# Optimization experiments

Measured on AMD Instinct MI355X. Metric: run time of the kernel, lower is better.

## Reference

```python
import jax, jax.numpy as jnp
import numpy as np

N_NODES, N_EDGES = 50000, 800000
NODE_D, MSG_D, OUT_D = 128, 128, 128


def _linear_params(key, d_in, d_out):
    kw, _ = jax.random.split(key)
    W = jax.random.normal(kw, (d_in, d_out), jnp.float32) * np.float32(1.0 / np.sqrt(d_in))
    b = jnp.zeros((d_out,), jnp.float32)
    return W, b


def setup_inputs() -> dict:
    key = jax.random.key(0)
    ks = jax.random.split(key, 12)
    node_features = jax.random.normal(ks[0], (N_NODES, NODE_D), jnp.float32)
    src = jax.random.randint(ks[1], (N_EDGES,), 0, N_NODES, dtype=jnp.int32)
    dst = jax.random.randint(ks[2], (N_EDGES,), 0, N_NODES, dtype=jnp.int32)
    W_msg_1, b_msg_1 = _linear_params(ks[3], NODE_D, MSG_D)
    W_msg_2, b_msg_2 = _linear_params(ks[4], MSG_D, MSG_D)
    W_msg_3, b_msg_3 = _linear_params(ks[5], MSG_D, MSG_D)
    W_att_1, b_att_1 = _linear_params(ks[6], 2 * NODE_D, 1)
    W_att_2, b_att_2 = _linear_params(ks[7], 2 * NODE_D, 1)
    W_att_3, b_att_3 = _linear_params(ks[8], 2 * NODE_D, 1)
    W_c1, b_c1 = _linear_params(ks[9], MSG_D + NODE_D, OUT_D)
    W_c2, b_c2 = _linear_params(ks[10], OUT_D, OUT_D)
    return {
        'node_features': node_features, 'src': src, 'dst': dst,
        'W_msg_1': W_msg_1, 'b_msg_1': b_msg_1,
        'W_msg_2': W_msg_2, 'b_msg_2': b_msg_2,
        'W_msg_3': W_msg_3, 'b_msg_3': b_msg_3,
        'W_att_1': W_att_1, 'b_att_1': b_att_1,
        'W_att_2': W_att_2, 'b_att_2': b_att_2,
        'W_att_3': W_att_3, 'b_att_3': b_att_3,
        'W_c1': W_c1, 'b_c1': b_c1,
        'W_c2': W_c2, 'b_c2': b_c2,
    }


def reference(node_features, src, dst,
              W_msg_1, b_msg_1, W_msg_2, b_msg_2, W_msg_3, b_msg_3,
              W_att_1, b_att_1, W_att_2, b_att_2, W_att_3, b_att_3,
              W_c1, b_c1, W_c2, b_c2):
    # dropout(0.2) is identity in eval mode
    h = node_features                     # [N, D]
    N = h.shape[0]
    hs = h[src]                           # [E, D] gather source features
    hd = h[dst]                           # [E, D] gather dest features
    e = jnp.concatenate([hs, hd], axis=1)  # [E, 2D]

    # three per-edge scalar attention heads: exp(relu(linear))
    a1 = jnp.exp(jax.nn.relu(e @ W_att_1 + b_att_1))  # [E, 1]
    a2 = jnp.exp(jax.nn.relu(e @ W_att_2 + b_att_2))
    a3 = jnp.exp(jax.nn.relu(e @ W_att_3 + b_att_3))

    # per-destination normalizers (segment sums over incoming edges)
    att1 = jax.ops.segment_sum(a1, dst, num_segments=N)  # [N, 1]
    att2 = jax.ops.segment_sum(a2, dst, num_segments=N)
    att3 = jax.ops.segment_sum(a3, dst, num_segments=N)

    avg_a = (a1 / att1[dst] + a2 / att2[dst] + a3 / att3[dst]) / 3.0  # [E, 1]

    # gathered 3-layer MLP message, scaled by averaged attention
    m = avg_a * jax.nn.relu(
        jax.nn.relu(jax.nn.relu(hs @ W_msg_1 + b_msg_1) @ W_msg_2 + b_msg_2) @ W_msg_3 + b_msg_3
    )  # [E, M]

    # mean over incoming edges (nodes with no in-edges get 0, like DGL)
    deg = jax.ops.segment_sum(jnp.ones((src.shape[0], 1), h.dtype), dst, num_segments=N)
    h_neigh = jax.ops.segment_sum(m, dst, num_segments=N) / jnp.maximum(deg, 1.0)  # [N, M]

    hc = jnp.concatenate([h, h_neigh], axis=1)  # [N, D+M]
    out = jax.nn.relu(hc @ W_c1 + b_c1) @ W_c2 + b_c2  # [N, O]
    return out
```

## Files before the change

### kernel.cpp

```cpp
#include <hip/hip_runtime.h>

#define NDIM 128
#define NWPART 128
#define MAXBKT 1024

typedef __attribute__((ext_vector_type(8))) short s8v;
typedef __attribute__((ext_vector_type(4))) float f4v;

__device__ inline unsigned short f2bf_rne(float x) {
    unsigned u = __float_as_uint(x);
    unsigned r = u + 0x7FFFu + ((u >> 16) & 1u);
    return (unsigned short)(r >> 16);
}
__device__ inline float bf2f(unsigned short b) {
    return __uint_as_float(((unsigned)b) << 16);
}

__global__ __launch_bounds__(256) void k_front(const float* __restrict__ h,
                                               const float* __restrict__ Wa1,
                                               const float* __restrict__ Wa2,
                                               const float* __restrict__ Wa3,
                                               float* __restrict__ proj,
                                               unsigned short* __restrict__ hb,
                                               const float* __restrict__ w0,
                                               const float* __restrict__ w1,
                                               const float* __restrict__ w2,
                                               const float* __restrict__ w3,
                                               const float* __restrict__ w4,
                                               const float* __restrict__ w5,
                                               unsigned short* __restrict__ wtout,
                                               const int* __restrict__ dst,
                                               int* __restrict__ hist,
                                               int N, int E, int nbkt)
{
    __shared__ int lh[MAXBKT];
    int tid = threadIdx.x;
    int nbProj = (N + 15) >> 4;
    int bid = blockIdx.x;

    if (bid < 384) {
        const float* srcs[6] = {w0, w1, w2, w3, w4, w5};
        int mat = bid >> 6;
        int idx = (bid & 63) * 256 + tid;
        int j    = idx & 7;
        int lane = (idx >> 3) & 63;
        int ks   = (idx >> 9) & 3;
        int ct   = idx >> 11;
        int col  = ct * 16 + (lane & 15);
        int k    = ks * 32 + (lane >> 4) * 8 + j;
        wtout[(size_t)mat * 16384 + idx] = f2bf_rne(srcs[mat][k * 128 + col]);
        return;
    }
    bid -= 384;
    if (bid < nbProj) {
        int l = tid & 15;
        int n = bid * 16 + (tid >> 4);
        if (n >= N) return;
        int o = l * 8;
        float4 w1s0 = *(const float4*)(Wa1 + o),       w1s1 = *(const float4*)(Wa1 + o + 4);
        float4 w1d0 = *(const float4*)(Wa1 + 128 + o), w1d1 = *(const float4*)(Wa1 + 132 + o);
        float4 w2s0 = *(const float4*)(Wa2 + o),       w2s1 = *(const float4*)(Wa2 + o + 4);
        float4 w2d0 = *(const float4*)(Wa2 + 128 + o), w2d1 = *(const float4*)(Wa2 + 132 + o);
        float4 w3s0 = *(const float4*)(Wa3 + o),       w3s1 = *(const float4*)(Wa3 + o + 4);
        float4 w3d0 = *(const float4*)(Wa3 + 128 + o), w3d1 = *(const float4*)(Wa3 + 132 + o);
        float4 x0 = *(const float4*)(h + (size_t)n * NDIM + o);
        float4 x1 = *(const float4*)(h + (size_t)n * NDIM + o + 4);
        {
            s8v hv;
            hv[0] = (short)f2bf_rne(x0.x); hv[1] = (short)f2bf_rne(x0.y);
            hv[2] = (short)f2bf_rne(x0.z); hv[3] = (short)f2bf_rne(x0.w);
            hv[4] = (short)f2bf_rne(x1.x); hv[5] = (short)f2bf_rne(x1.y);
            hv[6] = (short)f2bf_rne(x1.z); hv[7] = (short)f2bf_rne(x1.w);
            *(s8v*)(hb + (size_t)n * NDIM + o) = hv;
        }
        float s1 = x0.x*w1s0.x + x0.y*w1s0.y + x0.z*w1s0.z + x0.w*w1s0.w
                 + x1.x*w1s1.x + x1.y*w1s1.y + x1.z*w1s1.z + x1.w*w1s1.w;
        float s2 = x0.x*w2s0.x + x0.y*w2s0.y + x0.z*w2s0.z + x0.w*w2s0.w
                 + x1.x*w2s1.x + x1.y*w2s1.y + x1.z*w2s1.z + x1.w*w2s1.w;
        float s3 = x0.x*w3s0.x + x0.y*w3s0.y + x0.z*w3s0.z + x0.w*w3s0.w
                 + x1.x*w3s1.x + x1.y*w3s1.y + x1.z*w3s1.z + x1.w*w3s1.w;
        float d1 = x0.x*w1d0.x + x0.y*w1d0.y + x0.z*w1d0.z + x0.w*w1d0.w
                 + x1.x*w1d1.x + x1.y*w1d1.y + x1.z*w1d1.z + x1.w*w1d1.w;
        float d2 = x0.x*w2d0.x + x0.y*w2d0.y + x0.z*w2d0.z + x0.w*w2d0.w
                 + x1.x*w2d1.x + x1.y*w2d1.y + x1.z*w2d1.z + x1.w*w2d1.w;
        float d3 = x0.x*w3d0.x + x0.y*w3d0.y + x0.z*w3d0.z + x0.w*w3d0.w
                 + x1.x*w3d1.x + x1.y*w3d1.y + x1.z*w3d1.z + x1.w*w3d1.w;
#pragma unroll
        for (int m = 1; m < 16; m <<= 1) {
            s1 += __shfl_xor(s1, m);
            s2 += __shfl_xor(s2, m);
            s3 += __shfl_xor(s3, m);
            d1 += __shfl_xor(d1, m);
            d2 += __shfl_xor(d2, m);
            d3 += __shfl_xor(d3, m);
        }
        if (l == 0) {
            *(float4*)(proj + (size_t)n * 8)     = make_float4(s1, s2, s3, 0.f);
            *(float4*)(proj + (size_t)n * 8 + 4) = make_float4(d1, d2, d3, 0.f);
        }
        return;
    }
    bid -= nbProj;
    {
        int w = bid, NW = NWPART;
        for (int i = tid; i < nbkt; i += 256) lh[i] = 0;
        __syncthreads();
        int per = (E + NW - 1) / NW;
        int e0 = w * per, e1 = min(E, e0 + per);
        for (int e = e0 + tid; e < e1; e += 256)
            atomicAdd(&lh[dst[e] >> 6], 1);
        __syncthreads();
        for (int b = tid; b < nbkt; b += 256)
            hist[b * NW + w] = lh[b];
    }
}

__global__ __launch_bounds__(NWPART) void k_pscan_a(int* __restrict__ hist,
                                                    int* __restrict__ tot)
{
    __shared__ int s[NWPART];
    int b = blockIdx.x, t = threadIdx.x;
    int v = hist[b * NWPART + t];
    s[t] = v;
    __syncthreads();
    for (int d = 1; d < NWPART; d <<= 1) {
        int u = (t >= d) ? s[t - d] : 0;
        __syncthreads();
        s[t] += u;
        __syncthreads();
    }
    hist[b * NWPART + t] = s[t] - v;
    if (t == NWPART - 1) tot[b] = s[NWPART - 1];
}

__global__ __launch_bounds__(MAXBKT) void k_pscan_b(const int* __restrict__ tot,
                                                    int* __restrict__ bbase,
                                                    int E, int nbkt)
{
    __shared__ int s[MAXBKT];
    int b = threadIdx.x;
    int v = (b < nbkt) ? tot[b] : 0;
    s[b] = v;
    __syncthreads();
    for (int d = 1; d < MAXBKT; d <<= 1) {
        int u = (b >= d) ? s[b - d] : 0;
        __syncthreads();
        s[b] += u;
        __syncthreads();
    }
    if (b < nbkt) bbase[b] = s[b] - v;
    if (b == nbkt - 1) bbase[nbkt] = E;
}


__device__ inline void g_pass_global(const unsigned short* __restrict__ A, int N, int row0,
                                     int ln, int g, int lane, int cw,
                                     const unsigned short* __restrict__ wf, f4v acc[2][2])
{
#pragma unroll
    for (int ks = 0; ks < 4; ++ks) {
        s8v a[2];
#pragma unroll
        for (int fr = 0; fr < 2; ++fr) {
            int rA = min(row0 + fr * 16 + ln, N - 1);
            a[fr] = *(const s8v*)(A + (size_t)rA * 128 + ks * 32 + g * 8);
        }
#pragma unroll
        for (int ct2 = 0; ct2 < 2; ++ct2) {
            int ct = cw * 2 + ct2;
            s8v wv = *(const s8v*)(wf + ((((ct << 2) + ks) * 64) + lane) * 8);
#pragma unroll
            for (int fr = 0; fr < 2; ++fr)
                acc[fr][ct2] = __builtin_amdgcn_mfma_f32_16x16x32_bf16(a[fr], wv, acc[fr][ct2], 0, 0, 0);
        }
    }
}

__device__ inline void g_pass_lds(const unsigned short* __restrict__ act,
                                  int rw, int ln, int g, int lane, int cw,
                                  const unsigned short* __restrict__ wf, f4v acc[2][2])
{
#pragma unroll
    for (int ks = 0; ks < 4; ++ks) {
        s8v a[2];
#pragma unroll
        for (int fr = 0; fr < 2; ++fr) {
            int rl = rw * 32 + fr * 16 + ln;
            a[fr] = *(const s8v*)(&act[(rl * 128 + ks * 32 + g * 8) ^ ((ln & 7) << 3)]);
        }
#pragma unroll
        for (int ct2 = 0; ct2 < 2; ++ct2) {
            int ct = cw * 2 + ct2;
            s8v wv = *(const s8v*)(wf + ((((ct << 2) + ks) * 64) + lane) * 8);
#pragma unroll
            for (int fr = 0; fr < 2; ++fr)
                acc[fr][ct2] = __builtin_amdgcn_mfma_f32_16x16x32_bf16(a[fr], wv, acc[fr][ct2], 0, 0, 0);
        }
    }
}

__device__ inline void write_act(f4v acc[2][2], const float* __restrict__ bias,
                                 unsigned short* __restrict__ act,
                                 int rw, int cw, int ln, int g)
{
#pragma unroll
    for (int ct2 = 0; ct2 < 2; ++ct2) {
        int col = (cw * 2 + ct2) * 16 + ln;
        float bv = bias[col];
#pragma unroll
        for (int fr = 0; fr < 2; ++fr) {
#pragma unroll
            for (int q = 0; q < 4; ++q) {
                int rl = rw * 32 + fr * 16 + g * 4 + q;
                float o = fmaxf(acc[fr][ct2][q] + bv, 0.f);
                act[(rl * 128 + col) ^ ((rl & 7) << 3)] = f2bf_rne(o);
                acc[fr][ct2][q] = 0.f;
            }
        }
    }
}

__global__ __launch_bounds__(512) void k_mid(const int* __restrict__ src,
                                             const int* __restrict__ dst,
                                             const int* __restrict__ hist,
                                             const int* __restrict__ bbase,
                                             unsigned* __restrict__ ebuf,
                                             int E, int nbkt,
                                             const unsigned short* __restrict__ hb,
                                             const unsigned short* __restrict__ w1,
                                             const unsigned short* __restrict__ w2,
                                             const unsigned short* __restrict__ w3,
                                             const float* __restrict__ b1,
                                             const float* __restrict__ b2,
                                             const float* __restrict__ b3,
                                             unsigned short* __restrict__ msg, int N)
{
    __shared__ int cur[MAXBKT];
    __shared__ unsigned short act0[8192];
    __shared__ unsigned short act1[8192];
    int tid = threadIdx.x;

    if (blockIdx.x < NWPART) {
        int w = blockIdx.x, NW = NWPART;
        for (int i = tid; i < nbkt; i += 512)
            cur[i] = hist[i * NW + w] + bbase[i];
        __syncthreads();
        int per = (E + NW - 1) / NW;
        int e0 = w * per, e1 = min(E, e0 + per);
        for (int e = e0 + tid; e < e1; e += 512) {
            int d = dst[e], b = d >> 6;
            int pos = atomicAdd(&cur[b], 1);
            ebuf[pos] = ((unsigned)src[e] << 7) | (unsigned)(d & 63);
        }
        return;
    }
    int mb   = blockIdx.x - NWPART;
    int lane = tid & 63;
    int wid  = tid >> 6;
    int rw   = wid >> 2;
    int cw   = wid & 3;
    int ln   = lane & 15;
    int g    = lane >> 4;
    int row0 = mb * 64 + rw * 32;

    f4v acc[2][2] = {};
    g_pass_global(hb, N, row0, ln, g, lane, cw, w1, acc);
    write_act(acc, b1, act0, rw, cw, ln, g);
    __syncthreads();
    g_pass_lds(act0, rw, ln, g, lane, cw, w2, acc);
    write_act(acc, b2, act1, rw, cw, ln, g);
    __syncthreads();
    g_pass_lds(act1, rw, ln, g, lane, cw, w3, acc);
    write_act(acc, b3, act0, rw, cw, ln, g);
    __syncthreads();
#pragma unroll
    for (int i = 0; i < 2; ++i) {
        int id  = tid + 512 * i;
        int row = id >> 4;
        int c8  = (id & 15) * 8;
        int grow = mb * 64 + row;
        if (grow < N) {
            s8v v = *(const s8v*)(&act0[(row * 128 + c8) ^ ((row & 7) << 3)]);
            *(s8v*)(msg + (size_t)grow * 128 + c8) = v;
        }
    }
}

__global__ __launch_bounds__(512) void k_tail(const unsigned short* __restrict__ hb,
                                              const unsigned short* __restrict__ msgb,
                                              const float* __restrict__ proj,
                                              const int* __restrict__ bbase,
                                              const unsigned* __restrict__ ebuf,
                                              const float* __restrict__ ba1,
                                              const float* __restrict__ ba2,
                                              const float* __restrict__ ba3,
                                              const unsigned short* __restrict__ wc1a,
                                              const unsigned short* __restrict__ wc1b,
                                              const unsigned short* __restrict__ wc2,
                                              const float* __restrict__ bc1,
                                              const float* __restrict__ bc2,
                                              float* __restrict__ out, int N)
{
    __shared__ unsigned short hn[8192];
    __shared__ unsigned short act0[8192];
    __shared__ int lperm[1536];
    __shared__ int lcnt[64];
    __shared__ int lsc[64];
    __shared__ int loffs[65];
    __shared__ int lcur[64];
    int tid  = threadIdx.x;
    int lane = tid & 63;
    int l    = lane & 15;
    int grp  = lane >> 4;
    int wv   = tid >> 6;
    int r0   = blockIdx.x * 64;
    float b1 = ba1[0], b2 = ba2[0], b3 = ba3[0];

    int be0 = bbase[blockIdx.x], be1 = bbase[blockIdx.x + 1];
    if (tid < 64) lcnt[tid] = 0;
    __syncthreads();
    for (int e = be0 + tid; e < be1; e += 512)
        atomicAdd(&lcnt[ebuf[e] & 63], 1);
    __syncthreads();
    if (tid < 64) lsc[tid] = lcnt[tid];
    __syncthreads();
    for (int d = 1; d < 64; d <<= 1) {
        int u = (tid < 64 && tid >= d) ? lsc[tid - d] : 0;
        __syncthreads();
        if (tid < 64) lsc[tid] += u;
        __syncthreads();
    }
    if (tid < 64) {
        int excl = lsc[tid] - lcnt[tid];
        loffs[tid] = excl;
        lcur[tid]  = excl;
        if (tid == 63) loffs[64] = lsc[63];
    }
    __syncthreads();
    for (int e = be0 + tid; e < be1; e += 512) {
        unsigned r = ebuf[e];
        int p = atomicAdd(&lcur[r & 63], 1);
        if (p < 1536) lperm[p] = (int)(r >> 7);
    }
    __syncthreads();

    for (int rnd = 0; rnd < 2; ++rnd) {
        int rl = rnd * 32 + wv * 4 + grp;
        int n  = r0 + rl;
        bool alive = (n < N);
        int o0 = loffs[rl], o1 = loffs[rl + 1];
        float dd1 = 0.f, dd2 = 0.f, dd3 = 0.f;
        if (alive) {
            dd1 = proj[(size_t)n * 8 + 4];
            dd2 = proj[(size_t)n * 8 + 5];
            dd3 = proj[(size_t)n * 8 + 6];
        }
        int deg = o1 - o0;

        int   m0 = min(deg, 16);
        int   sc = 0;
        float a1c = 0.f, a2c = 0.f, a3c = 0.f;
        if (l < m0) {
            sc = lperm[o0 + l];
            float4 sp = *(const float4*)(proj + (size_t)sc * 8);
            a1c = __expf(fmaxf(sp.x + dd1 + b1, 0.f));
            a2c = __expf(fmaxf(sp.y + dd2 + b2, 0.f));
            a3c = __expf(fmaxf(sp.z + dd3 + b3, 0.f));
        }
        float s1 = a1c, s2 = a2c, s3 = a3c;
        for (int i = o0 + 16 + l; i < o1; i += 16) {
            int s = lperm[i];
            float4 sp = *(const float4*)(proj + (size_t)s * 8);
            s1 += __expf(fmaxf(sp.x + dd1 + b1, 0.f));
            s2 += __expf(fmaxf(sp.y + dd2 + b2, 0.f));
            s3 += __expf(fmaxf(sp.z + dd3 + b3, 0.f));
        }
#pragma unroll
        for (int m = 1; m < 16; m <<= 1) {
            s1 += __shfl_xor(s1, m);
            s2 += __shfl_xor(s2, m);
            s3 += __shfl_xor(s3, m);
        }
        float r1 = 1.f / s1, r2 = 1.f / s2, r3 = 1.f / s3;

        float acc[8] = {};
        int gbase = grp << 4;
        {
            float wvv = (a1c * r1 + a2c * r2 + a3c * r3) * (1.f / 3.f);
            for (int j = 0; j < m0; ++j) {
                int   s = __shfl(sc, gbase + j);
                float w = __shfl(wvv, gbase + j);
                s8v v = *(const s8v*)(msgb + (size_t)s * NDIM + l * 8);
#pragma unroll
                for (int k = 0; k < 8; ++k)
                    acc[k] += w * bf2f((unsigned short)v[k]);
            }
        }
        for (int base = o0 + 16; base < o1; base += 16) {
            int m  = min(16, o1 - base);
            int sv = 0;
            float wvv = 0.f;
            if (l < m) {
                sv = lperm[base + l];
                float4 sp = *(const float4*)(proj + (size_t)sv * 8);
                float a1 = __expf(fmaxf(sp.x + dd1 + b1, 0.f));
                float a2 = __expf(fmaxf(sp.y + dd2 + b2, 0.f));
                float a3 = __expf(fmaxf(sp.z + dd3 + b3, 0.f));
                wvv = (a1 * r1 + a2 * r2 + a3 * r3) * (1.f / 3.f);
            }
            for (int j = 0; j < m; ++j) {
                int   s = __shfl(sv, gbase + j);
                float w = __shfl(wvv, gbase + j);
                s8v v = *(const s8v*)(msgb + (size_t)s * NDIM + l * 8);
#pragma unroll
                for (int k = 0; k < 8; ++k)
                    acc[k] += w * bf2f((unsigned short)v[k]);
            }
        }
        float inv = (alive && deg > 0) ? 1.f / (float)deg : 0.f;
        s8v hv;
#pragma unroll
        for (int k = 0; k < 8; ++k)
            hv[k] = (short)f2bf_rne(acc[k] * inv);
        *(s8v*)(&hn[(rl * 128 + l * 8) ^ ((rl & 7) << 3)]) = hv;
    }
    __syncthreads();

    int wid  = tid >> 6;
    int rw   = wid >> 2;
    int cw   = wid & 3;
    int ln   = lane & 15;
    int g    = lane >> 4;
    int row0 = r0 + rw * 32;

    f4v acc2[2][2] = {};
    g_pass_global(hb, N, row0, ln, g, lane, cw, wc1a, acc2);
    g_pass_lds(hn, rw, ln, g, lane, cw, wc1b, acc2);
    write_act(acc2, bc1, act0, rw, cw, ln, g);
    __syncthreads();
    g_pass_lds(act0, rw, ln, g, lane, cw, wc2, acc2);
#pragma unroll
    for (int ct2 = 0; ct2 < 2; ++ct2) {
        int col = (cw * 2 + ct2) * 16 + ln;
        float bv = bc2[col];
#pragma unroll
        for (int fr = 0; fr < 2; ++fr) {
#pragma unroll
            for (int q = 0; q < 4; ++q) {
                int orow = row0 + fr * 16 + g * 4 + q;
                if (orow < N)
                    out[(size_t)orow * 128 + col] = acc2[fr][ct2][q] + bv;
            }
        }
    }
}

extern "C" void kernel_launch(void* const* d_in, const int* in_sizes, int n_in,
                              void* d_out, int out_size, void* d_ws, size_t ws_size,
                              hipStream_t stream)
{
    const float* h   = (const float*)d_in[0];
    const int*   src = (const int*)d_in[1];
    const int*   dst = (const int*)d_in[2];
    const float* Wm1 = (const float*)d_in[3];
    const float* bm1 = (const float*)d_in[4];
    const float* Wm2 = (const float*)d_in[5];
    const float* bm2 = (const float*)d_in[6];
    const float* Wm3 = (const float*)d_in[7];
    const float* bm3 = (const float*)d_in[8];
    const float* Wa1 = (const float*)d_in[9];
    const float* ba1 = (const float*)d_in[10];
    const float* Wa2 = (const float*)d_in[11];
    const float* ba2 = (const float*)d_in[12];
    const float* Wa3 = (const float*)d_in[13];
    const float* ba3 = (const float*)d_in[14];
    const float* Wc1 = (const float*)d_in[15];
    const float* bc1 = (const float*)d_in[16];
    const float* Wc2 = (const float*)d_in[17];
    const float* bc2 = (const float*)d_in[18];

    const int N = in_sizes[0] / NDIM;
    const int E = in_sizes[1];
    const int nbkt = (N + 63) >> 6;
    float* out = (float*)d_out;

    unsigned short* wt  = (unsigned short*)d_ws;
    unsigned short* hb  = wt + 6 * 16384;
    unsigned short* mb2 = hb + (size_t)N * NDIM;
    float* proj = (float*)(mb2 + (size_t)N * NDIM);
    int* hist   = (int*)(proj + (size_t)N * 8);
    int* bbase  = hist + MAXBKT * NWPART;
    int* btot   = bbase + MAXBKT + 1;
    unsigned* ebuf = (unsigned*)(btot + MAXBKT);

    const unsigned short* wt_m1  = wt;
    const unsigned short* wt_m2  = wt + 1 * 16384;
    const unsigned short* wt_m3  = wt + 2 * 16384;
    const unsigned short* wt_c1a = wt + 3 * 16384;
    const unsigned short* wt_c1b = wt + 4 * 16384;
    const unsigned short* wt_c2  = wt + 5 * 16384;

    int nbProj = (N + 15) / 16;
    int gb64   = nbkt;

    k_front<<<384 + nbProj + NWPART, 256, 0, stream>>>(
        h, Wa1, Wa2, Wa3, proj, hb,
        Wm1, Wm2, Wm3, Wc1, Wc1 + 128 * 128, Wc2, wt,
        dst, hist, N, E, nbkt);

    k_pscan_a<<<nbkt, NWPART, 0, stream>>>(hist, btot);
    k_pscan_b<<<1, MAXBKT, 0, stream>>>(btot, bbase, E, nbkt);

    k_mid<<<NWPART + gb64, 512, 0, stream>>>(
        src, dst, hist, bbase, ebuf, E, nbkt,
        hb, wt_m1, wt_m2, wt_m3, bm1, bm2, bm3, mb2, N);

    k_tail<<<gb64, 512, 0, stream>>>(
        hb, mb2, proj, bbase, ebuf, ba1, ba2, ba3,
        wt_c1a, wt_c1b, wt_c2, bc1, bc2, out, N);
}
```

Baseline: 101.1 us.

## Stage gathered message rows into LDS via global_load_lds, one wave per node

The neighbor aggregation now gives each destination node a whole wave instead of a 16-lane group. It issues direct global-to-LDS loads (global_load_lds) of up to 16 source message rows into a per-wave staging buffer, waits on vmcnt, then accumulates two bf16 channels per lane from LDS. Attention normalizers are now computed with 64 lanes per node. The aim is more memory-level parallelism in the irregular gather and less register pressure. The cost is 32KB of extra LDS, which may lower occupancy, and nodes are handled serially per wave with a full wait per chunk, so there is no overlap between loading and accumulating.

```diff
diff --git a/kernel.cpp b/kernel.cpp
--- a/kernel.cpp
+++ b/kernel.cpp
@@ -15,6 +15,11 @@
 __device__ inline float bf2f(unsigned short b) {
     return __uint_as_float(((unsigned)b) << 16);
 }
+
+#define GLOAD_LDS(gaddr, laddr)                                                        \
+    __builtin_amdgcn_global_load_lds(                                                  \
+        (const __attribute__((address_space(1))) unsigned int*)(gaddr),                \
+        (__attribute__((address_space(3))) unsigned int*)(laddr), 4, 0, 0)
 
 __global__ __launch_bounds__(256) void k_front(const float* __restrict__ h,
                                                const float* __restrict__ Wa1,
@@ -308,10 +313,9 @@
     __shared__ int lsc[64];
     __shared__ int loffs[65];
     __shared__ int lcur[64];
+    __shared__ unsigned char stage[8][4096];
     int tid  = threadIdx.x;
     int lane = tid & 63;
-    int l    = lane & 15;
-    int grp  = lane >> 4;
     int wv   = tid >> 6;
     int r0   = blockIdx.x * 64;
     float b1 = ba1[0], b2 = ba2[0], b3 = ba3[0];
@@ -344,85 +348,86 @@
     }
     __syncthreads();
 
-    for (int rnd = 0; rnd < 2; ++rnd) {
-        int rl = rnd * 32 + wv * 4 + grp;
+    unsigned char* stg = stage[wv];
+    for (int i = 0; i < 8; ++i) {
+        int rl = wv * 8 + i;
         int n  = r0 + rl;
         bool alive = (n < N);
         int o0 = loffs[rl], o1 = loffs[rl + 1];
+        int deg = alive ? (o1 - o0) : 0;
+
+        int c0 = min(deg, 16);
+        for (int j = 0; j < c0; ++j) {
+            int s = lperm[o0 + j];
+            GLOAD_LDS((const char*)(msgb + (size_t)s * NDIM) + lane * 4, stg + j * 256);
+        }
+
         float dd1 = 0.f, dd2 = 0.f, dd3 = 0.f;
         if (alive) {
             dd1 = proj[(size_t)n * 8 + 4];
             dd2 = proj[(size_t)n * 8 + 5];
             dd3 = proj[(size_t)n * 8 + 6];
         }
-        int deg = o1 - o0;
-
-        int   m0 = min(deg, 16);
+        int m64 = min(deg, 64);
         int   sc = 0;
         float a1c = 0.f, a2c = 0.f, a3c = 0.f;
-        if (l < m0) {
-            sc = lperm[o0 + l];
+        if (lane < m64) {
+            sc = lperm[o0 + lane];
             float4 sp = *(const float4*)(proj + (size_t)sc * 8);
             a1c = __expf(fmaxf(sp.x + dd1 + b1, 0.f));
             a2c = __expf(fmaxf(sp.y + dd2 + b2, 0.f));
             a3c = __expf(fmaxf(sp.z + dd3 + b3, 0.f));
         }
         float s1 = a1c, s2 = a2c, s3 = a3c;
-        for (int i = o0 + 16 + l; i < o1; i += 16) {
-            int s = lperm[i];
+        for (int e = o0 + 64 + lane; e < o1; e += 64) {
+            int s = lperm[e];
             float4 sp = *(const float4*)(proj + (size_t)s * 8);
             s1 += __expf(fmaxf(sp.x + dd1 + b1, 0.f));
             s2 += __expf(fmaxf(sp.y + dd2 + b2, 0.f));
             s3 += __expf(fmaxf(sp.z + dd3 + b3, 0.f));
         }
 #pragma unroll
-        for (int m = 1; m < 16; m <<= 1) {
+        for (int m = 1; m < 64; m <<= 1) {
             s1 += __shfl_xor(s1, m);
             s2 += __shfl_xor(s2, m);
             s3 += __shfl_xor(s3, m);
         }
         float r1 = 1.f / s1, r2 = 1.f / s2, r3 = 1.f / s3;
-
-        float acc[8] = {};
-        int gbase = grp << 4;
-        {
-            float wvv = (a1c * r1 + a2c * r2 + a3c * r3) * (1.f / 3.f);
-            for (int j = 0; j < m0; ++j) {
-                int   s = __shfl(sc, gbase + j);
-                float w = __shfl(wvv, gbase + j);
-                s8v v = *(const s8v*)(msgb + (size_t)s * NDIM + l * 8);
-#pragma unroll
-                for (int k = 0; k < 8; ++k)
-                    acc[k] += w * bf2f((unsigned short)v[k]);
+        float wlane = (lane < m64) ? (a1c * r1 + a2c * r2 + a3c * r3) * (1.f / 3.f) : 0.f;
+
+        float accx = 0.f, accy = 0.f;
+        for (int base = 0; base < deg; base += 16) {
+            int m = min(16, deg - base);
+            if (base > 0) {
+                for (int j = 0; j < m; ++j) {
+                    int s = lperm[o0 + base + j];
+                    GLOAD_LDS((const char*)(msgb + (size_t)s * NDIM) + lane * 4, stg + j * 256);
+                }
             }
-        }
-        for (int base = o0 + 16; base < o1; base += 16) {
-            int m  = min(16, o1 - base);
-            int sv = 0;
-            float wvv = 0.f;
-            if (l < m) {
-                sv = lperm[base + l];
-                float4 sp = *(const float4*)(proj + (size_t)sv * 8);
-                float a1 = __expf(fmaxf(sp.x + dd1 + b1, 0.f));
-                float a2 = __expf(fmaxf(sp.y + dd2 + b2, 0.f));
-                float a3 = __expf(fmaxf(sp.z + dd3 + b3, 0.f));
-                wvv = (a1 * r1 + a2 * r2 + a3 * r3) * (1.f / 3.f);
+            asm volatile("s_waitcnt vmcnt(0)" ::: "memory");
+            for (int j = 0; j < m; ++j) {
+                int ej = base + j;
+                float w;
+                if (ej < 64) {
+                    w = __shfl(wlane, ej);
+                } else {
+                    int s = lperm[o0 + ej];
+                    float4 sp = *(const float4*)(proj + (size_t)s * 8);
+                    float a1 = __expf(fmaxf(sp.x + dd1 + b1, 0.f));
+                    float a2 = __expf(fmaxf(sp.y + dd2 + b2, 0.f));
+                    float a3 = __expf(fmaxf(sp.z + dd3 + b3, 0.f));
+                    w = (a1 * r1 + a2 * r2 + a3 * r3) * (1.f / 3.f);
+                }
+                ushort2 v = *(const ushort2*)(stg + j * 256 + lane * 4);
+                accx += w * bf2f(v.x);
+                accy += w * bf2f(v.y);
             }
-            for (int j = 0; j < m; ++j) {
-                int   s = __shfl(sv, gbase + j);
-                float w = __shfl(wvv, gbase + j);
-                s8v v = *(const s8v*)(msgb + (size_t)s * NDIM + l * 8);
-#pragma unroll
-                for (int k = 0; k < 8; ++k)
-                    acc[k] += w * bf2f((unsigned short)v[k]);
-            }
-        }
-        float inv = (alive && deg > 0) ? 1.f / (float)deg : 0.f;
-        s8v hv;
-#pragma unroll
-        for (int k = 0; k < 8; ++k)
-            hv[k] = (short)f2bf_rne(acc[k] * inv);
-        *(s8v*)(&hn[(rl * 128 + l * 8) ^ ((rl & 7) << 3)]) = hv;
+        }
+        float inv = (deg > 0) ? 1.f / (float)deg : 0.f;
+        ushort2 hv;
+        hv.x = f2bf_rne(accx * inv);
+        hv.y = f2bf_rne(accy * inv);
+        *(ushort2*)(&hn[(rl * 128 + lane * 2) ^ ((rl & 7) << 3)]) = hv;
     }
     __syncthreads();
 
```

New measurement: 134.0 us. 32.6% more time.
